# Optimization experiments

Hardware: AMD Instinct MI355X
Metric: run time of the kernel (lower is better)

The kernel has to match this reference:

```python
import jax, jax.numpy as jnp
import numpy as np

B, S, D, H = 256, 64, 1024, 16
DH = D // H          # 64
BOARD = 8
NREL = 2 * (BOARD - 1) + 1  # 15


def _rel_indices():
    # Relative row/col offsets between all pairs of board squares, shifted to [0, 2*(BOARD-1)]
    coords = np.arange(S)
    row = coords // BOARD
    col = coords % BOARD
    rr = row[:, None] - row[None, :] + (BOARD - 1)  # (S, S)
    rc = col[:, None] - col[None, :] + (BOARD - 1)  # (S, S)
    return jnp.asarray(rr), jnp.asarray(rc)


def setup_inputs() -> dict:
    key = jax.random.key(0)
    ks = jax.random.split(key, 12)
    p = lambda k, sh: jax.random.normal(k, sh, jnp.float32) * 0.02
    return {
        "x": jax.random.normal(ks[0], (B, S, D), jnp.float32),
        "wq": p(ks[1], (D, D)),
        "wk": p(ks[2], (D, D)),
        "wv": p(ks[3], (D, D)),
        "wo": p(ks[4], (D, D)),
        "bo": jnp.zeros((D,), jnp.float32),
        "eq_h": p(ks[5], (NREL, DH)),
        "eq_w": p(ks[6], (NREL, DH)),
        "ek_h": p(ks[7], (NREL, DH)),
        "ek_w": p(ks[8], (NREL, DH)),
        "ev_h": p(ks[9], (NREL, DH)),
        "ev_w": p(ks[10], (NREL, DH)),
    }


def reference(x, wq, wk, wv, wo, bo, eq_h, eq_w, ek_h, ek_w, ev_h, ev_w):
    rr, rc = _rel_indices()
    rel_q = eq_h[rr] + eq_w[rc]  # (S, S, DH)
    rel_k = ek_h[rr] + ek_w[rc]
    rel_v = ev_h[rr] + ev_w[rc]

    def heads(y):
        return y.reshape(B, S, H, DH).transpose(0, 2, 1, 3)  # (B, H, S, DH)

    q = heads(x @ wq.T)
    k = heads(x @ wk.T)
    v = heads(x @ wv.T)

    # (q_i + rq_ij) . (k_j + rk_ij), expanded to avoid the (B,H,S,S,DH) intermediates
    scores = (
        jnp.einsum('bhid,bhjd->bhij', q, k)
        + jnp.einsum('bhid,ijd->bhij', q, rel_k)
        + jnp.einsum('ijd,bhjd->bhij', rel_q, k)
        + jnp.sum(rel_q * rel_k, axis=-1)[None, None]
    )
    attn = jax.nn.softmax(scores / jnp.sqrt(jnp.float32(DH)), axis=-1)  # (B, H, S, S)

    # sum_j attn_ij * (v_j + rv_ij)
    ctx = (
        jnp.einsum('bhij,bhjd->bhid', attn, v)
        + jnp.einsum('bhij,ijd->bhid', attn, rel_v)
    )
    ctx = ctx.transpose(0, 2, 1, 3).reshape(B, S, D)
    return ctx @ wo.T + bo
```

## Files before the change

kernel.cpp:

```cpp
#include <hip/hip_runtime.h>
#include <hip/hip_bf16.h>

typedef __hip_bfloat16 bf16;
typedef __attribute__((ext_vector_type(8))) short short8;
typedef __attribute__((ext_vector_type(8))) unsigned short ushort8;
typedef __attribute__((ext_vector_type(4))) float floatx4;

__device__ __forceinline__ short f2s(float x) {
  bf16 h = __float2bfloat16(x);
  short s;
  __builtin_memcpy(&s, &h, 2);
  return s;
}

__device__ __forceinline__ void gl_lds16(const bf16* g, bf16* l) {
  __builtin_amdgcn_global_load_lds(
      (const __attribute__((address_space(1))) unsigned int*)g,
      (__attribute__((address_space(3))) unsigned int*)l, 16, 0, 0);
}

#define MFMA16(a, b, c) __builtin_amdgcn_mfma_f32_16x16x32_bf16((a), (b), (c), 0, 0, 0)

__device__ __forceinline__ void bar() {
  asm volatile("" ::: "memory");
  __builtin_amdgcn_s_barrier();
  asm volatile("" ::: "memory");
}

#define VMCNT(N) asm volatile("s_waitcnt vmcnt(" #N ")" ::: "memory")

__device__ __forceinline__ void cvt8(const float* s, bf16* dst) {
  float4 a = *(const float4*)s;
  float4 b = *(const float4*)(s + 4);
  short8 r;
  r[0] = f2s(a.x); r[1] = f2s(a.y); r[2] = f2s(a.z); r[3] = f2s(a.w);
  r[4] = f2s(b.x); r[5] = f2s(b.y); r[6] = f2s(b.z); r[7] = f2s(b.w);
  *(short8*)dst = r;
}

__global__ __launch_bounds__(256) void convert_f32_bf16(
    const float* __restrict__ src, bf16* __restrict__ dst, int n) {
  const int i = (blockIdx.x * 256 + threadIdx.x) * 8;
  if (i + 7 < n) cvt8(src + i, dst + i);
}

__global__ __launch_bounds__(256) void convert_all(
    const float* __restrict__ x,  bf16* __restrict__ xb,
    const float* __restrict__ wq, bf16* __restrict__ wqb,
    const float* __restrict__ wk, bf16* __restrict__ wkb,
    const float* __restrict__ wv, bf16* __restrict__ wvb,
    const float* __restrict__ wo, bf16* __restrict__ wob,
    const float* __restrict__ eqh, const float* __restrict__ eqw,
    const float* __restrict__ ekh, const float* __restrict__ ekw,
    const float* __restrict__ evh, const float* __restrict__ evw,
    bf16* __restrict__ ews, float* __restrict__ S4f)
{
  const int b = blockIdx.x;
  const int t = threadIdx.x;
  if (b < 8192) {
    const int i = (b * 256 + t) * 8;
    cvt8(x + i, xb + i);
    return;
  }
  if (b < 10240) {
    const int wsel = (b - 8192) >> 9;
    const int i = (((b - 8192) & 511) * 256 + t) * 8;
    const float* s = (wsel == 0) ? wq : (wsel == 1) ? wk : (wsel == 2) ? wv : wo;
    bf16* d = (wsel == 0) ? wqb : (wsel == 1) ? wkb : (wsel == 2) ? wvb : wob;
    cvt8(s + i, d + i);
    return;
  }
  if (t < 96) {
    const int tb = t >> 4, row = t & 15;
    const float* src[6] = {eqh, eqw, ekh, ekw, evh, evw};
    bf16* dst = ews + tb * 1024 + row * 64;
    if (row < 15) {
      const float* s = src[tb] + row * 64;
      #pragma unroll
      for (int d = 0; d < 64; d += 8) cvt8(s + d, dst + d);
    } else {
      const short8 z = {0, 0, 0, 0, 0, 0, 0, 0};
      #pragma unroll
      for (int d = 0; d < 64; d += 8) *(short8*)(dst + d) = z;
    }
  }
  if (t < 225) {
    const int r = t / 15, c = t % 15;
    float s = 0.f;
    for (int d = 0; d < 64; ++d)
      s += (eqh[r * 64 + d] + eqw[c * 64 + d]) * (ekh[r * 64 + d] + ekw[c * 64 + d]);
    S4f[t] = s;
  }
}

__global__ __launch_bounds__(256) void precompute_tables(
    const float* __restrict__ eqh, const float* __restrict__ eqw,
    const float* __restrict__ ekh, const float* __restrict__ ekw,
    const float* __restrict__ evh, const float* __restrict__ evw,
    bf16* __restrict__ ews, float* __restrict__ S4f)
{
  const int t = threadIdx.x;
  if (t < 96) {
    const int tb = t >> 4, row = t & 15;
    const float* src[6] = {eqh, eqw, ekh, ekw, evh, evw};
    bf16* dst = ews + tb * 1024 + row * 64;
    if (row < 15) {
      const float* s = src[tb] + row * 64;
      #pragma unroll
      for (int d = 0; d < 64; d += 8) cvt8(s + d, dst + d);
    } else {
      const short8 z = {0, 0, 0, 0, 0, 0, 0, 0};
      #pragma unroll
      for (int d = 0; d < 64; d += 8) *(short8*)(dst + d) = z;
    }
  }
  if (t < 225) {
    const int r = t / 15, c = t % 15;
    float s = 0.f;
    for (int d = 0; d < 64; ++d)
      s += (eqh[r * 64 + d] + eqw[c * 64 + d]) * (ekh[r * 64 + d] + ekw[c * 64 + d]);
    S4f[t] = s;
  }
}

template <int TAG>
__global__ __launch_bounds__(512, 2) void gemm256(
    const bf16* __restrict__ A,
    const bf16* __restrict__ W0, const bf16* __restrict__ W1, const bf16* __restrict__ W2,
    const float* __restrict__ bias, int hasBias,
    bf16* __restrict__ O0, bf16* __restrict__ O1, bf16* __restrict__ O2,
    float* __restrict__ Ofp, int outF32)
{
  __shared__ bf16 lds[65536];

  const int nx = gridDim.x;
  const int orig = blockIdx.y * nx + blockIdx.x;
  const int xcd = orig & 7;
  const int c = orig >> 3;
  const int bxp = nx >> 3;
  const int bx = xcd * bxp + (c % bxp);
  const int by = c / bxp;

  const int m0 = bx * 256;
  const int which = by >> 2;
  const bf16* W = (which == 0) ? W0 : (which == 1) ? W1 : W2;
  bf16* O = (which == 0) ? O0 : (which == 1) ? O1 : O2;
  const int n0 = (by & 3) * 256;

  const int t = threadIdx.x;
  const int lane = t & 63, w = t >> 6;
  const int wm = w >> 2, wn = w & 3;
  const int quad = lane >> 4, n16 = lane & 15;

  const int srow = (t >> 6) * 16 + ((t & 63) >> 2);
  const int scol = ((t & 3) * 8) ^ (((t >> 5) & 1) << 4);
  const bf16* Abase = A + (m0 + srow) * 1024 + scol;
  const bf16* Bbase = W + (n0 + srow) * 1024 + scol;
  const int wdst = w * 512;

  const int swzq = (quad * 8) ^ ((n16 >> 3) << 4);
  const int aoff = wm * 4096 + n16 * 32 + swzq;
  const int boff = wn * 2048 + n16 * 32 + swzq;

  floatx4 acc[8][4];
  const floatx4 zero4 = {0.f, 0.f, 0.f, 0.f};
  #pragma unroll
  for (int mi = 0; mi < 8; ++mi)
    #pragma unroll
    for (int ni = 0; ni < 4; ++ni) acc[mi][ni] = zero4;

  #pragma unroll
  for (int p = 0; p < 3; ++p) {
    const bf16* ga = Abase + p * 32;
    bf16* la = lds + p * 16384 + wdst;
    gl_lds16(ga, la); gl_lds16(ga + 131072, la + 4096);
    const bf16* gb = Bbase + p * 32;
    bf16* lb = lds + p * 16384 + 8192 + wdst;
    gl_lds16(gb, lb); gl_lds16(gb + 131072, lb + 4096);
  }
  VMCNT(8);
  bar();

#define TILE_STEP(TT, DOSTAGE, WAITSEQ) do {                                   \
    const bf16* bA_ = lds + ((TT) & 3) * 16384;                                \
    const bf16* bB_ = bA_ + 8192;                                              \
    short8 af_[4], bq_[4];                                                     \
    _Pragma("unroll")                                                          \
    for (int mi = 0; mi < 4; ++mi)                                             \
      af_[mi] = *(const short8*)(bA_ + aoff + mi * 512);                       \
    _Pragma("unroll")                                                          \
    for (int ni = 0; ni < 4; ++ni)                                             \
      bq_[ni] = *(const short8*)(bB_ + boff + ni * 512);                       \
    if (DOSTAGE) {                                                             \
      const bf16* g_ = Abase + ((TT) + 3) * 32;                                \
      bf16* l_ = lds + (((TT) + 3) & 3) * 16384 + wdst;                        \
      gl_lds16(g_, l_); gl_lds16(g_ + 131072, l_ + 4096);                      \
    }                                                                          \
    __builtin_amdgcn_s_setprio(1);                                             \
    _Pragma("unroll")                                                          \
    for (int mi = 0; mi < 4; ++mi)                                             \
      _Pragma("unroll")                                                        \
      for (int ni = 0; ni < 4; ++ni)                                           \
        acc[mi][ni] = MFMA16(af_[mi], bq_[ni], acc[mi][ni]);                   \
    __builtin_amdgcn_s_setprio(0);                                             \
    _Pragma("unroll")                                                          \
    for (int mi = 0; mi < 4; ++mi)                                             \
      af_[mi] = *(const short8*)(bA_ + aoff + 2048 + mi * 512);                \
    if (DOSTAGE) {                                                             \
      const bf16* g_ = Bbase + ((TT) + 3) * 32;                                \
      bf16* l_ = lds + (((TT) + 3) & 3) * 16384 + 8192 + wdst;                 \
      gl_lds16(g_, l_); gl_lds16(g_ + 131072, l_ + 4096);                      \
    }                                                                          \
    __builtin_amdgcn_s_setprio(1);                                             \
    _Pragma("unroll")                                                          \
    for (int mi = 0; mi < 4; ++mi)                                             \
      _Pragma("unroll")                                                        \
      for (int ni = 0; ni < 4; ++ni)                                           \
        acc[mi + 4][ni] = MFMA16(af_[mi], bq_[ni], acc[mi + 4][ni]);           \
    __builtin_amdgcn_s_setprio(0);                                             \
    WAITSEQ;                                                                   \
  } while (0)

  #pragma unroll 1
  for (int tt = 0; tt < 29; ++tt) {
    TILE_STEP(tt, 1, VMCNT(8); bar());
  }
  TILE_STEP(29, 0, VMCNT(4); bar());
  TILE_STEP(30, 0, VMCNT(0); bar());
  TILE_STEP(31, 0, (void)0);
#undef TILE_STEP

  float bvv[4];
  #pragma unroll
  for (int ni = 0; ni < 4; ++ni)
    bvv[ni] = hasBias ? bias[n0 + wn * 64 + ni * 16 + n16] : 0.f;
  #pragma unroll
  for (int mi = 0; mi < 8; ++mi) {
    #pragma unroll
    for (int r = 0; r < 4; ++r) {
      const int row = m0 + wm * 128 + mi * 16 + quad * 4 + r;
      if (outF32) {
        #pragma unroll
        for (int ni = 0; ni < 4; ++ni)
          Ofp[row * 1024 + n0 + wn * 64 + ni * 16 + n16] = acc[mi][ni][r] + bvv[ni];
      } else {
        #pragma unroll
        for (int ni = 0; ni < 4; ++ni)
          O[row * 1024 + n0 + wn * 64 + ni * 16 + n16] =
              __float2bfloat16(acc[mi][ni][r] + bvv[ni]);
      }
    }
  }
}

template <int TAG>
__global__ __launch_bounds__(256) void gemm_bt(
    const bf16* __restrict__ A,
    const void* __restrict__ W0, const void* __restrict__ W1, const void* __restrict__ W2,
    int wBf,
    const float* __restrict__ bias, int hasBias,
    bf16* __restrict__ O0, bf16* __restrict__ O1, bf16* __restrict__ O2,
    float* __restrict__ Ofp, int outF32)
{
  __shared__ bf16 As[128 * 64];
  __shared__ bf16 Bs[128 * 64];

  const int m0 = blockIdx.x * 128;
  const int by = blockIdx.y;
  const int which = by >> 3;
  const void* W = (which == 0) ? W0 : (which == 1) ? W1 : W2;
  bf16* O = (which == 0) ? O0 : (which == 1) ? O1 : O2;
  const int n0 = (by & 7) * 128;

  const int t = threadIdx.x;
  const int lane = t & 63, w = t >> 6;
  const int lrow = lane >> 3, lcol = (lane & 7) * 8;
  const int wm = w >> 1, wn = w & 1;
  const int quad = lane >> 4, n16 = lane & 15;

  const int swzA = ((lrow & 1) << 5) | (((lrow >> 1) & 3) << 3);
  const int gcol = lcol ^ swzA;
  const int swzR = ((n16 & 1) << 5) | (((n16 >> 1) & 3) << 3);

  floatx4 acc[4][4];
  const floatx4 zero4 = {0.f, 0.f, 0.f, 0.f};
  #pragma unroll
  for (int mi = 0; mi < 4; ++mi)
    #pragma unroll
    for (int ni = 0; ni < 4; ++ni) acc[mi][ni] = zero4;

  const int arowb = m0 + w * 32 + lrow;
  const int browb = n0 + w * 32 + lrow;
  bf16* lau = As + w * 2048;
  bf16* lbu = Bs + w * 2048;

  if (wBf) {
    const bf16* Wb = (const bf16*)W;
    for (int k0 = 0; k0 < 1024; k0 += 64) {
      if (k0) __syncthreads();
      const bf16* ga = A + arowb * 1024 + k0 + gcol;
      const bf16* gw = Wb + browb * 1024 + k0 + gcol;
      #pragma unroll
      for (int c = 0; c < 4; ++c) {
        gl_lds16(ga + c * 8192, lau + c * 512);
        gl_lds16(gw + c * 8192, lbu + c * 512);
      }
      __syncthreads();
      #pragma unroll
      for (int ks = 0; ks < 2; ++ks) {
        short8 af[4], bfv[4];
        #pragma unroll
        for (int mi = 0; mi < 4; ++mi)
          af[mi] = *(const short8*)(As + (wm * 64 + mi * 16 + n16) * 64 +
                                    ((ks * 32 + quad * 8) ^ swzR));
        #pragma unroll
        for (int ni = 0; ni < 4; ++ni)
          bfv[ni] = *(const short8*)(Bs + (wn * 64 + ni * 16 + n16) * 64 +
                                     ((ks * 32 + quad * 8) ^ swzR));
        #pragma unroll
        for (int mi = 0; mi < 4; ++mi)
          #pragma unroll
          for (int ni = 0; ni < 4; ++ni)
            acc[mi][ni] = MFMA16(af[mi], bfv[ni], acc[mi][ni]);
      }
    }
  } else {
    const float* Wf = (const float*)W;
    for (int k0 = 0; k0 < 1024; k0 += 64) {
      short8 rb[4];
      #pragma unroll
      for (int c = 0; c < 4; ++c) {
        const float* f = Wf + (browb + c * 8) * 1024 + k0 + gcol;
        float4 a = *(const float4*)f;
        float4 b = *(const float4*)(f + 4);
        short8 r;
        r[0] = f2s(a.x); r[1] = f2s(a.y); r[2] = f2s(a.z); r[3] = f2s(a.w);
        r[4] = f2s(b.x); r[5] = f2s(b.y); r[6] = f2s(b.z); r[7] = f2s(b.w);
        rb[c] = r;
      }
      if (k0) __syncthreads();
      const bf16* ga = A + arowb * 1024 + k0 + gcol;
      #pragma unroll
      for (int c = 0; c < 4; ++c) {
        gl_lds16(ga + c * 8192, lau + c * 512);
        *(short8*)(lbu + lane * 8 + c * 512) = rb[c];
      }
      __syncthreads();
      #pragma unroll
      for (int ks = 0; ks < 2; ++ks) {
        short8 af[4], bfv[4];
        #pragma unroll
        for (int mi = 0; mi < 4; ++mi)
          af[mi] = *(const short8*)(As + (wm * 64 + mi * 16 + n16) * 64 +
                                    ((ks * 32 + quad * 8) ^ swzR));
        #pragma unroll
        for (int ni = 0; ni < 4; ++ni)
          bfv[ni] = *(const short8*)(Bs + (wn * 64 + ni * 16 + n16) * 64 +
                                     ((ks * 32 + quad * 8) ^ swzR));
        #pragma unroll
        for (int mi = 0; mi < 4; ++mi)
          #pragma unroll
          for (int ni = 0; ni < 4; ++ni)
            acc[mi][ni] = MFMA16(af[mi], bfv[ni], acc[mi][ni]);
      }
    }
  }

  #pragma unroll
  for (int ni = 0; ni < 4; ++ni) {
    const int col = n0 + wn * 64 + ni * 16 + n16;
    const float bv = hasBias ? bias[col] : 0.f;
    #pragma unroll
    for (int mi = 0; mi < 4; ++mi) {
      #pragma unroll
      for (int r = 0; r < 4; ++r) {
        const int row = m0 + wm * 64 + mi * 16 + quad * 4 + r;
        if (outF32) Ofp[row * 1024 + col] = acc[mi][ni][r] + bv;
        else        O[row * 1024 + col] = __float2bfloat16(acc[mi][ni][r] + bv);
      }
    }
  }
}

__global__ __launch_bounds__(256, 3) void attn_rel(
    const bf16* __restrict__ Q, const bf16* __restrict__ Km, const bf16* __restrict__ V,
    const bf16* __restrict__ ews, const float* __restrict__ S4f,
    bf16* __restrict__ Ctx)
{
  __shared__ bf16 vT[64][106];
  __shared__ bf16 pa[64][104];
  __shared__ float Ahs[64][16], Aws[64][16];
  __shared__ float Bhs[15][64], Bws[15][64];
  __shared__ float S4s[225];

  const int t = threadIdx.x;
  const int b = blockIdx.x >> 4, h = blockIdx.x & 15;
  const int base = b * 65536 + h * 64;
  const int lane = t & 63, w = t >> 6;
  const int quad = lane >> 4, n16 = lane & 15;

  const bf16* qrow = Q + base + (w * 16 + n16) * 1024 + quad * 8;
  short8 aq0 = *(const short8*)(qrow);
  short8 aq1 = *(const short8*)(qrow + 32);
  short8 bk0[4], bk1[4];
  #pragma unroll
  for (int nj = 0; nj < 4; ++nj) {
    const bf16* krow = Km + base + (nj * 16 + n16) * 1024 + quad * 8;
    bk0[nj] = *(const short8*)(krow);
    bk1[nj] = *(const short8*)(krow + 32);
  }
  short8 ebf[4][2];
  #pragma unroll
  for (int tb = 0; tb < 4; ++tb) {
    const bf16* er = ews + tb * 1024 + n16 * 64 + quad * 8;
    ebf[tb][0] = *(const short8*)(er);
    ebf[tb][1] = *(const short8*)(er + 32);
  }

  {
    const int r = t >> 2, c0 = (t & 3) * 16;
    const bf16* vrow = V + base + r * 1024 + c0;
    int4 v0 = *(const int4*)(vrow);
    int4 v1 = *(const int4*)(vrow + 8);
    const unsigned short* p0 = (const unsigned short*)&v0;
    const unsigned short* p1 = (const unsigned short*)&v1;
    #pragma unroll
    for (int ii = 0; ii < 8; ++ii) {
      *(unsigned short*)&vT[c0 + ii][r] = p0[ii];
      *(unsigned short*)&vT[c0 + 8 + ii][r] = p1[ii];
    }
    if (t < 60) {
      const int r2 = t >> 2, d0 = (t & 3) * 16;
      ushort8 pe0 = *(const ushort8*)(ews + 4096 + r2 * 64 + d0);
      ushort8 pe1 = *(const ushort8*)(ews + 4096 + r2 * 64 + d0 + 8);
      ushort8 pf0 = *(const ushort8*)(ews + 5120 + r2 * 64 + d0);
      ushort8 pf1 = *(const ushort8*)(ews + 5120 + r2 * 64 + d0 + 8);
      #pragma unroll
      for (int ii = 0; ii < 8; ++ii) {
        *(unsigned short*)&vT[d0 + ii][64 + r2] = pe0[ii];
        *(unsigned short*)&vT[d0 + 8 + ii][64 + r2] = pe1[ii];
        *(unsigned short*)&vT[d0 + ii][79 + r2] = pf0[ii];
        *(unsigned short*)&vT[d0 + 8 + ii][79 + r2] = pf1[ii];
      }
    }
    if (t < 64) {
      *(unsigned short*)&vT[t][94] = 0; *(unsigned short*)&vT[t][95] = 0;
      *(unsigned short*)&pa[t][94] = 0; *(unsigned short*)&pa[t][95] = 0;
    }
    if (t < 225) S4s[t] = S4f[t];
  }

  floatx4 cqk[4];
  #pragma unroll
  for (int nj = 0; nj < 4; ++nj) {
    floatx4 c = {0.f, 0.f, 0.f, 0.f};
    c = MFMA16(aq0, bk0[nj], c);
    c = MFMA16(aq1, bk1[nj], c);
    cqk[nj] = c;
  }
  {
    floatx4 cah = {0.f, 0.f, 0.f, 0.f}, caw = cah, cbh = cah, cbw = cah;
    cah = MFMA16(aq0, ebf[2][0], cah); cah = MFMA16(aq1, ebf[2][1], cah);
    caw = MFMA16(aq0, ebf[3][0], caw); caw = MFMA16(aq1, ebf[3][1], caw);
    cbh = MFMA16(bk0[w], ebf[0][0], cbh); cbh = MFMA16(bk1[w], ebf[0][1], cbh);
    cbw = MFMA16(bk0[w], ebf[1][0], cbw); cbw = MFMA16(bk1[w], ebf[1][1], cbw);
    #pragma unroll
    for (int r = 0; r < 4; ++r) {
      const int i = w * 16 + quad * 4 + r;
      Ahs[i][n16] = cah[r];
      Aws[i][n16] = caw[r];
      if (n16 < 15) { Bhs[n16][i] = cbh[r]; Bws[n16][i] = cbw[r]; }
    }
  }
  __syncthreads();

  const int i_base = w * 16 + quad * 4;
  float xv[4][4];
  #pragma unroll
  for (int nj = 0; nj < 4; ++nj) {
    const int j = nj * 16 + n16;
    const int rowj = j >> 3, colj = j & 7;
    #pragma unroll
    for (int r = 0; r < 4; ++r) {
      const int i = i_base + r;
      const int rowi = i >> 3, coli = i & 7;
      const int rr = rowi - rowj + 7, rc = coli - colj + 7;
      xv[r][nj] = (cqk[nj][r] + Ahs[i][rr] + Aws[i][rc] + Bhs[rr][j] + Bws[rc][j]
                   + S4s[rr * 15 + rc]) * 0.125f;
    }
  }
  #pragma unroll
  for (int r = 0; r < 4; ++r) {
    const int i = i_base + r;
    const int rowi = i >> 3, coli = i & 7;
    float mx = fmaxf(fmaxf(xv[r][0], xv[r][1]), fmaxf(xv[r][2], xv[r][3]));
    #pragma unroll
    for (int off = 1; off < 16; off <<= 1) mx = fmaxf(mx, __shfl_xor(mx, off));
    float p[4];
    float sm = 0.f;
    #pragma unroll
    for (int nj = 0; nj < 4; ++nj) { p[nj] = __expf(xv[r][nj] - mx); sm += p[nj]; }
    #pragma unroll
    for (int off = 1; off < 16; off <<= 1) sm += __shfl_xor(sm, off);
    const float inv = 1.0f / sm;
    #pragma unroll
    for (int nj = 0; nj < 4; ++nj) {
      p[nj] *= inv;
      pa[i][nj * 16 + n16] = __float2bfloat16(p[nj]);
    }
    float ph[4];
    #pragma unroll
    for (int nj = 0; nj < 4; ++nj) {
      float v = p[nj];
      v += __shfl_xor(v, 1); v += __shfl_xor(v, 2); v += __shfl_xor(v, 4);
      ph[nj] = v;
    }
    float s4 = p[0] + p[1] + p[2] + p[3];
    float pw = s4 + __shfl_xor(s4, 8);
    if ((n16 & 7) == 0) {
      const int hh = n16 >> 3;
      #pragma unroll
      for (int nj = 0; nj < 4; ++nj) {
        const int g = nj * 2 + hh;
        pa[i][64 + rowi + 7 - g] = __float2bfloat16(ph[nj]);
      }
    } else if (n16 < 8) {
      const int z = n16 - 1;
      pa[i][64 + (z < rowi ? z : z + 8)] = __float2bfloat16(0.f);
    }
    if (n16 < 8) {
      pa[i][79 + coli + 7 - n16] = __float2bfloat16(pw);
    } else {
      const int z = n16 - 8;
      pa[i][79 + (z < coli ? z : z + 8)] = __float2bfloat16(0.f);
    }
  }
  __threadfence_block();

  short8 ap[3];
  #pragma unroll
  for (int ksb = 0; ksb < 3; ++ksb)
    ap[ksb] = *(const short8*)&pa[w * 16 + n16][ksb * 32 + quad * 8];
  #pragma unroll
  for (int nj = 0; nj < 4; ++nj) {
    floatx4 c = {0.f, 0.f, 0.f, 0.f};
    #pragma unroll
    for (int ksb = 0; ksb < 3; ++ksb) {
      short8 bv = *(const short8*)&vT[nj * 16 + n16][ksb * 32 + quad * 8];
      c = MFMA16(ap[ksb], bv, c);
    }
    #pragma unroll
    for (int r = 0; r < 4; ++r) {
      const int i = i_base + r;
      Ctx[base + i * 1024 + nj * 16 + n16] = __float2bfloat16(c[r]);
    }
  }
}

extern "C" void kernel_launch(void* const* d_in, const int* in_sizes, int n_in,
                              void* d_out, int out_size, void* d_ws, size_t ws_size,
                              hipStream_t stream) {
  const float* x   = (const float*)d_in[0];
  const float* wq  = (const float*)d_in[1];
  const float* wk  = (const float*)d_in[2];
  const float* wv  = (const float*)d_in[3];
  const float* wo  = (const float*)d_in[4];
  const float* bo  = (const float*)d_in[5];
  const float* eqh = (const float*)d_in[6];
  const float* eqw = (const float*)d_in[7];
  const float* ekh = (const float*)d_in[8];
  const float* ekw = (const float*)d_in[9];
  const float* evh = (const float*)d_in[10];
  const float* evw = (const float*)d_in[11];
  float* outf = (float*)d_out;

  const size_t hdr = (ws_size - 16384) & ~(size_t)1023;
  bf16* ewsB = (bf16*)((char*)d_ws + hdr);
  float* S4f = (float*)((char*)d_ws + hdr + 12288);

  if (ws_size >= (size_t)73 * 1024 * 1024) {
    bf16* qb = (bf16*)d_ws;
    bf16* kb = qb + 16777216;
    bf16* wqb = kb + 16777216;
    bf16* wkb = wqb + 1048576;
    bf16* wvb = wkb + 1048576;
    bf16* wob = wvb + 1048576;
    bf16* xb = (bf16*)d_out;
    bf16* vb = (bf16*)((char*)d_out + 33554432);

    convert_all<<<10241, 256, 0, stream>>>(
        x, xb, wq, wqb, wk, wkb, wv, wvb, wo, wob,
        eqh, eqw, ekh, ekw, evh, evw, ewsB, S4f);

    gemm256<0><<<dim3(64, 12), 512, 0, stream>>>(
        xb, wqb, wkb, wvb, nullptr, 0, qb, kb, vb, nullptr, 0);
    attn_rel<<<dim3(4096), 256, 0, stream>>>(qb, kb, vb, ewsB, S4f, qb);
    gemm256<1><<<dim3(64, 4), 512, 0, stream>>>(
        qb, wob, nullptr, nullptr, bo, 1, nullptr, nullptr, nullptr, outf, 1);
  } else {
    precompute_tables<<<1, 256, 0, stream>>>(eqh, eqw, ekh, ekw, evh, evw, ewsB, S4f);
    bf16* xb0 = (bf16*)((char*)d_out + 16777216);
    bf16* xb1 = (bf16*)((char*)d_out + 50331648);
    bf16* vQ2 = (bf16*)((char*)d_out + 33554432);
    bf16* qb = (bf16*)d_ws;
    bf16* kb = qb + 8388608;
    const int fastW = (ws_size >= (size_t)42 * 1024 * 1024) ? 1 : 0;
    bf16* wqb = kb + 8388608;
    bf16* wkb = wqb + 1048576;
    bf16* wvb = wkb + 1048576;
    bf16* wob = wvb + 1048576;

    convert_f32_bf16<<<4096, 256, 0, stream>>>(x, xb0, 8388608);
    convert_f32_bf16<<<4096, 256, 0, stream>>>(x + 8388608, xb1, 8388608);
    if (fastW) {
      convert_f32_bf16<<<512, 256, 0, stream>>>(wq, wqb, 1048576);
      convert_f32_bf16<<<512, 256, 0, stream>>>(wk, wkb, 1048576);
      convert_f32_bf16<<<512, 256, 0, stream>>>(wv, wvb, 1048576);
      convert_f32_bf16<<<512, 256, 0, stream>>>(wo, wob, 1048576);
    }

    for (int hh = 0; hh < 2; ++hh) {
      const bf16* xh = hh ? xb1 : xb0;
      if (fastW) {
        gemm256<0><<<dim3(32, 12), 512, 0, stream>>>(
            xh, wqb, wkb, wvb, nullptr, 0, qb, kb, vQ2, nullptr, 0);
      } else {
        gemm_bt<0><<<dim3(64, 24), 256, 0, stream>>>(
            xh, (const void*)wq, (const void*)wk, (const void*)wv,
            0, nullptr, 0, qb, kb, vQ2, nullptr, 0);
      }
      attn_rel<<<dim3(2048), 256, 0, stream>>>(qb, kb, vQ2, ewsB, S4f, qb);
      if (fastW) {
        gemm256<1><<<dim3(32, 4), 512, 0, stream>>>(
            qb, wob, nullptr, nullptr, bo, 1, nullptr, nullptr, nullptr,
            outf + (size_t)hh * 8388608, 1);
      } else {
        gemm_bt<1><<<dim3(64, 8), 256, 0, stream>>>(
            qb, (const void*)wo, nullptr, nullptr,
            0, bo, 1, nullptr, nullptr, nullptr,
            outf + (size_t)hh * 8388608, 1);
      }
    }
  }
}
```

Measured before the change: 350.4 us.

## Replace 256x256 GEMM tile with 128x128 tile, 3-stage pipeline

The 512-thread 256x256 GEMM becomes a 256-thread 128x128 kernel with a 3-slot LDS ring (48KB) and launch bounds allowing 3 blocks per CU. Grids are scaled up to match. The aim is more concurrent blocks and better latency hiding and tail balance, at the cost of half the arithmetic intensity per tile and more global/L2 traffic. The attention epilogue is also reordered so each row's four column stores are issued together.

Measured after the change: 358.6 us. +2.4%, slower.

```diff
diff --git a/kernel.cpp b/kernel.cpp
--- a/kernel.cpp
+++ b/kernel.cpp
@@ -124,14 +124,14 @@
 }
 
 template <int TAG>
-__global__ __launch_bounds__(512, 2) void gemm256(
+__global__ __launch_bounds__(256, 3) void gemm128(
     const bf16* __restrict__ A,
     const bf16* __restrict__ W0, const bf16* __restrict__ W1, const bf16* __restrict__ W2,
     const float* __restrict__ bias, int hasBias,
     bf16* __restrict__ O0, bf16* __restrict__ O1, bf16* __restrict__ O2,
     float* __restrict__ Ofp, int outF32)
 {
-  __shared__ bf16 lds[65536];
+  __shared__ bf16 lds[24576];
 
   const int nx = gridDim.x;
   const int orig = blockIdx.y * nx + blockIdx.x;
@@ -141,49 +141,53 @@
   const int bx = xcd * bxp + (c % bxp);
   const int by = c / bxp;
 
-  const int m0 = bx * 256;
-  const int which = by >> 2;
+  const int m0 = bx * 128;
+  const int which = by >> 3;
   const bf16* W = (which == 0) ? W0 : (which == 1) ? W1 : W2;
   bf16* O = (which == 0) ? O0 : (which == 1) ? O1 : O2;
-  const int n0 = (by & 3) * 256;
+  const int n0 = (by & 7) * 128;
 
   const int t = threadIdx.x;
   const int lane = t & 63, w = t >> 6;
-  const int wm = w >> 2, wn = w & 3;
+  const int wm = w >> 1, wn = w & 1;
   const int quad = lane >> 4, n16 = lane & 15;
 
-  const int srow = (t >> 6) * 16 + ((t & 63) >> 2);
+  const int srow = (t >> 6) * 16 + ((t >> 2) & 15);
   const int scol = ((t & 3) * 8) ^ (((t >> 5) & 1) << 4);
   const bf16* Abase = A + (m0 + srow) * 1024 + scol;
   const bf16* Bbase = W + (n0 + srow) * 1024 + scol;
   const int wdst = w * 512;
 
   const int swzq = (quad * 8) ^ ((n16 >> 3) << 4);
-  const int aoff = wm * 4096 + n16 * 32 + swzq;
+  const int aoff = wm * 2048 + n16 * 32 + swzq;
   const int boff = wn * 2048 + n16 * 32 + swzq;
 
-  floatx4 acc[8][4];
+  floatx4 acc[4][4];
   const floatx4 zero4 = {0.f, 0.f, 0.f, 0.f};
   #pragma unroll
-  for (int mi = 0; mi < 8; ++mi)
+  for (int mi = 0; mi < 4; ++mi)
     #pragma unroll
     for (int ni = 0; ni < 4; ++ni) acc[mi][ni] = zero4;
 
-  #pragma unroll
-  for (int p = 0; p < 3; ++p) {
-    const bf16* ga = Abase + p * 32;
-    bf16* la = lds + p * 16384 + wdst;
-    gl_lds16(ga, la); gl_lds16(ga + 131072, la + 4096);
-    const bf16* gb = Bbase + p * 32;
-    bf16* lb = lds + p * 16384 + 8192 + wdst;
-    gl_lds16(gb, lb); gl_lds16(gb + 131072, lb + 4096);
-  }
-  VMCNT(8);
+#define STAGE128(TT, SL) do {                                                  \
+    const bf16* gA_ = Abase + (TT) * 32;                                       \
+    const bf16* gB_ = Bbase + (TT) * 32;                                       \
+    bf16* lA_ = lds + (SL) * 8192 + wdst;                                      \
+    bf16* lB_ = lA_ + 4096;                                                    \
+    gl_lds16(gA_,         lA_);                                                \
+    gl_lds16(gA_ + 65536, lA_ + 2048);                                         \
+    gl_lds16(gB_,         lB_);                                                \
+    gl_lds16(gB_ + 65536, lB_ + 2048);                                         \
+  } while (0)
+
+  STAGE128(0, 0);
+  STAGE128(1, 1);
+  VMCNT(4);
   bar();
 
-#define TILE_STEP(TT, DOSTAGE, WAITSEQ) do {                                   \
-    const bf16* bA_ = lds + ((TT) & 3) * 16384;                                \
-    const bf16* bB_ = bA_ + 8192;                                              \
+#define STEP128(TT, SL, STSL, DOSTAGE, WAITSEQ) do {                           \
+    const bf16* bA_ = lds + (SL) * 8192;                                       \
+    const bf16* bB_ = bA_ + 4096;                                              \
     short8 af_[4], bq_[4];                                                     \
     _Pragma("unroll")                                                          \
     for (int mi = 0; mi < 4; ++mi)                                             \
@@ -191,11 +195,7 @@
     _Pragma("unroll")                                                          \
     for (int ni = 0; ni < 4; ++ni)                                             \
       bq_[ni] = *(const short8*)(bB_ + boff + ni * 512);                       \
-    if (DOSTAGE) {                                                             \
-      const bf16* g_ = Abase + ((TT) + 3) * 32;                                \
-      bf16* l_ = lds + (((TT) + 3) & 3) * 16384 + wdst;                        \
-      gl_lds16(g_, l_); gl_lds16(g_ + 131072, l_ + 4096);                      \
-    }                                                                          \
+    if (DOSTAGE) STAGE128((TT) + 2, STSL);                                     \
     __builtin_amdgcn_s_setprio(1);                                             \
     _Pragma("unroll")                                                          \
     for (int mi = 0; mi < 4; ++mi)                                             \
@@ -203,42 +203,30 @@
       for (int ni = 0; ni < 4; ++ni)                                           \
         acc[mi][ni] = MFMA16(af_[mi], bq_[ni], acc[mi][ni]);                   \
     __builtin_amdgcn_s_setprio(0);                                             \
-    _Pragma("unroll")                                                          \
-    for (int mi = 0; mi < 4; ++mi)                                             \
-      af_[mi] = *(const short8*)(bA_ + aoff + 2048 + mi * 512);                \
-    if (DOSTAGE) {                                                             \
-      const bf16* g_ = Bbase + ((TT) + 3) * 32;                                \
-      bf16* l_ = lds + (((TT) + 3) & 3) * 16384 + 8192 + wdst;                 \
-      gl_lds16(g_, l_); gl_lds16(g_ + 131072, l_ + 4096);                      \
-    }                                                                          \
-    __builtin_amdgcn_s_setprio(1);                                             \
-    _Pragma("unroll")                                                          \
-    for (int mi = 0; mi < 4; ++mi)                                             \
-      _Pragma("unroll")                                                        \
-      for (int ni = 0; ni < 4; ++ni)                                           \
-        acc[mi + 4][ni] = MFMA16(af_[mi], bq_[ni], acc[mi + 4][ni]);           \
-    __builtin_amdgcn_s_setprio(0);                                             \
     WAITSEQ;                                                                   \
   } while (0)
 
   #pragma unroll 1
-  for (int tt = 0; tt < 29; ++tt) {
-    TILE_STEP(tt, 1, VMCNT(8); bar());
-  }
-  TILE_STEP(29, 0, VMCNT(4); bar());
-  TILE_STEP(30, 0, VMCNT(0); bar());
-  TILE_STEP(31, 0, (void)0);
-#undef TILE_STEP
+  for (int g = 0; g < 10; ++g) {
+    const int tt = g * 3;
+    STEP128(tt,     0, 2, 1, VMCNT(4); bar());
+    STEP128(tt + 1, 1, 0, 1, VMCNT(4); bar());
+    STEP128(tt + 2, 2, 1, 1, VMCNT(4); bar());
+  }
+  STEP128(30, 0, 0, 0, VMCNT(0); bar());
+  STEP128(31, 1, 0, 0, (void)0);
+#undef STEP128
+#undef STAGE128
 
   float bvv[4];
   #pragma unroll
   for (int ni = 0; ni < 4; ++ni)
     bvv[ni] = hasBias ? bias[n0 + wn * 64 + ni * 16 + n16] : 0.f;
   #pragma unroll
-  for (int mi = 0; mi < 8; ++mi) {
+  for (int mi = 0; mi < 4; ++mi) {
     #pragma unroll
     for (int r = 0; r < 4; ++r) {
-      const int row = m0 + wm * 128 + mi * 16 + quad * 4 + r;
+      const int row = m0 + wm * 64 + mi * 16 + quad * 4 + r;
       if (outF32) {
         #pragma unroll
         for (int ni = 0; ni < 4; ++ni)
@@ -541,6 +529,7 @@
   #pragma unroll
   for (int ksb = 0; ksb < 3; ++ksb)
     ap[ksb] = *(const short8*)&pa[w * 16 + n16][ksb * 32 + quad * 8];
+  floatx4 cc[4];
   #pragma unroll
   for (int nj = 0; nj < 4; ++nj) {
     floatx4 c = {0.f, 0.f, 0.f, 0.f};
@@ -549,11 +538,14 @@
       short8 bv = *(const short8*)&vT[nj * 16 + n16][ksb * 32 + quad * 8];
       c = MFMA16(ap[ksb], bv, c);
     }
-    #pragma unroll
-    for (int r = 0; r < 4; ++r) {
-      const int i = i_base + r;
-      Ctx[base + i * 1024 + nj * 16 + n16] = __float2bfloat16(c[r]);
-    }
+    cc[nj] = c;
+  }
+  #pragma unroll
+  for (int r = 0; r < 4; ++r) {
+    const int i = i_base + r;
+    #pragma unroll
+    for (int nj = 0; nj < 4; ++nj)
+      Ctx[base + i * 1024 + nj * 16 + n16] = __float2bfloat16(cc[nj][r]);
   }
 }
 
@@ -592,10 +584,10 @@
         x, xb, wq, wqb, wk, wkb, wv, wvb, wo, wob,
         eqh, eqw, ekh, ekw, evh, evw, ewsB, S4f);
 
-    gemm256<0><<<dim3(64, 12), 512, 0, stream>>>(
+    gemm128<0><<<dim3(128, 24), 256, 0, stream>>>(
         xb, wqb, wkb, wvb, nullptr, 0, qb, kb, vb, nullptr, 0);
     attn_rel<<<dim3(4096), 256, 0, stream>>>(qb, kb, vb, ewsB, S4f, qb);
-    gemm256<1><<<dim3(64, 4), 512, 0, stream>>>(
+    gemm128<1><<<dim3(128, 8), 256, 0, stream>>>(
         qb, wob, nullptr, nullptr, bo, 1, nullptr, nullptr, nullptr, outf, 1);
   } else {
     precompute_tables<<<1, 256, 0, stream>>>(eqh, eqw, ekh, ekw, evh, evw, ewsB, S4f);
@@ -622,7 +614,7 @@
     for (int hh = 0; hh < 2; ++hh) {
       const bf16* xh = hh ? xb1 : xb0;
       if (fastW) {
-        gemm256<0><<<dim3(32, 12), 512, 0, stream>>>(
+        gemm128<0><<<dim3(64, 24), 256, 0, stream>>>(
             xh, wqb, wkb, wvb, nullptr, 0, qb, kb, vQ2, nullptr, 0);
       } else {
         gemm_bt<0><<<dim3(64, 24), 256, 0, stream>>>(
@@ -631,7 +623,7 @@
       }
       attn_rel<<<dim3(2048), 256, 0, stream>>>(qb, kb, vQ2, ewsB, S4f, qb);
       if (fastW) {
-        gemm256<1><<<dim3(32, 4), 512, 0, stream>>>(
+        gemm128<1><<<dim3(64, 8), 256, 0, stream>>>(
             qb, wob, nullptr, nullptr, bo, 1, nullptr, nullptr, nullptr,
             outf + (size_t)hh * 8388608, 1);
       } else {
```
